# Kernel tuning notes

Measured on AMD Instinct MI355X. Metric: run time of the kernel, lower is better.

Reference implementation:

```python
import jax, jax.numpy as jnp
import numpy as np

N_NODES = 100000


def gcn_layer(x, src, dst, W, b):
    # Standard torch_geometric GCNConv: add self-loops, symmetric deg^-1/2 norm,
    # linear transform, scatter-add aggregation, bias.
    n = x.shape[0]
    h = x @ W                                   # [N, out]
    loop = jnp.arange(n)
    s = jnp.concatenate([src, loop])            # [E+N]
    d = jnp.concatenate([dst, loop])
    deg = jax.ops.segment_sum(jnp.ones_like(d, dtype=h.dtype), d, num_segments=n)
    dinv = jax.lax.rsqrt(jnp.maximum(deg, 1.0)) # deg>=1 thanks to self-loops
    norm = dinv[s] * dinv[d]                    # [E+N]
    out = jax.ops.segment_sum(h[s] * norm[:, None], d, num_segments=n)
    return out + b


def setup_inputs() -> dict:
    key = jax.random.key(0)
    ks = jax.random.split(key, 8)
    N, E, IN, H, A = N_NODES, 1600000, 128, 128, 16
    x = jax.random.normal(ks[0], (N, IN), dtype=jnp.float32)
    edge_index = jax.random.randint(ks[1], (2, E), 0, N, dtype=jnp.int64)
    sc = lambda fi, fo: 1.0 / np.sqrt(fi)
    W1 = jax.random.normal(ks[2], (IN, H), dtype=jnp.float32) * sc(IN, H)
    b1 = jnp.zeros((H,), dtype=jnp.float32)
    W2 = jax.random.normal(ks[3], (H, H), dtype=jnp.float32) * sc(H, H)
    b2 = jnp.zeros((H,), dtype=jnp.float32)
    Wm = jax.random.normal(ks[4], (H, A), dtype=jnp.float32) * sc(H, A)
    bm = jnp.zeros((A,), dtype=jnp.float32)
    Ws = jax.random.normal(ks[5], (H, A), dtype=jnp.float32) * sc(H, A)
    bs = jnp.zeros((A,), dtype=jnp.float32)
    return {"x": x, "edge_index": edge_index, "W1": W1, "b1": b1,
            "W2": W2, "b2": b2, "Wm": Wm, "bm": bm, "Ws": Ws, "bs": bs}


def reference(x, edge_index, W1, b1, W2, b2, Wm, bm, Ws, bs):
    src, dst = edge_index[0], edge_index[1]
    h = jax.nn.relu(gcn_layer(x, src, dst, W1, b1))
    h = jax.nn.relu(gcn_layer(h, src, dst, W2, b2))
    mean = h @ Wm + bm
    logstd = h @ Ws + bs
    return (mean, logstd)
```

## Files before the change

kernel.cpp:

```cpp
#include <hip/hip_runtime.h>
#include <hip/hip_bf16.h>
#include <stdint.h>

static __device__ __forceinline__ ushort f2bf(float f){
  uint u = __float_as_uint(f);
  uint r = (u + 0x7fffu + ((u >> 16) & 1u)) >> 16;
  return (ushort)r;
}
static __device__ __forceinline__ float bf_lo(uint v){ return __uint_as_float(v << 16); }
static __device__ __forceinline__ float bf_hi(uint v){ return __uint_as_float(v & 0xffff0000u); }



__global__ __launch_bounds__(256) void k_bcount(const int* __restrict__ dst, int E, int CH,
                                                int* __restrict__ bcnt){
  __shared__ int hist[1024];
  for (int i = threadIdx.x; i < 1024; i += 256) hist[i] = 0;
  __syncthreads();
  int begin = blockIdx.x * CH;
  int end   = min(begin + CH, E);
  int i0 = begin + threadIdx.x * 4;
  for (int i = i0; i + 4 <= end; i += 1024){
    int4 d4 = *(const int4*)&dst[i];
    atomicAdd(&hist[d4.x >> 7], 1);
    atomicAdd(&hist[d4.y >> 7], 1);
    atomicAdd(&hist[d4.z >> 7], 1);
    atomicAdd(&hist[d4.w >> 7], 1);
  }
  int tailStart = begin + ((end - begin) & ~3);
  if (tailStart < end && threadIdx.x < (end - tailStart)){
    atomicAdd(&hist[dst[tailStart + threadIdx.x] >> 7], 1);
  }
  __syncthreads();
  for (int b = threadIdx.x; b < 1024; b += 256){
    int h = hist[b];
    if (h) atomicAdd(&bcnt[b], h);
  }
}


__global__ __launch_bounds__(256) void k_bscan(const int* __restrict__ bcnt, int* __restrict__ boff,
                                               int* __restrict__ bcur, int E){
  __shared__ int sh[256];
  int t = threadIdx.x, base = t * 4;
  int v0 = bcnt[base], v1 = bcnt[base+1], v2 = bcnt[base+2], v3 = bcnt[base+3];
  int s = v0 + v1 + v2 + v3;
  sh[t] = s; __syncthreads();
  for (int off = 1; off < 256; off <<= 1){
    int x = (t >= off) ? sh[t-off] : 0;
    __syncthreads(); sh[t] += x; __syncthreads();
  }
  int run = sh[t] - s;
  boff[base]   = run; bcur[base]   = run; run += v0;
  boff[base+1] = run; bcur[base+1] = run; run += v1;
  boff[base+2] = run; bcur[base+2] = run; run += v2;
  boff[base+3] = run; bcur[base+3] = run; run += v3;
  if (t == 255) boff[1024] = E;
}


__global__ __launch_bounds__(256) void k_bscatter(const int* __restrict__ src, const int* __restrict__ dst,
                                                  int E, int CH, int* __restrict__ bcur,
                                                  uint* __restrict__ ebuf){
  __shared__ int hist[1024];
  __shared__ int basea[1024];
  __shared__ int cnt[1024];
  for (int i = threadIdx.x; i < 1024; i += 256){ hist[i] = 0; cnt[i] = 0; }
  __syncthreads();
  int begin = blockIdx.x * CH;
  int end   = min(begin + CH, E);
  int i0 = begin + threadIdx.x * 4;
  for (int i = i0; i + 4 <= end; i += 1024){
    int4 d4 = *(const int4*)&dst[i];
    atomicAdd(&hist[d4.x >> 7], 1);
    atomicAdd(&hist[d4.y >> 7], 1);
    atomicAdd(&hist[d4.z >> 7], 1);
    atomicAdd(&hist[d4.w >> 7], 1);
  }
  int tailStart = begin + ((end - begin) & ~3);
  if (tailStart < end && threadIdx.x < (end - tailStart)){
    atomicAdd(&hist[dst[tailStart + threadIdx.x] >> 7], 1);
  }
  __syncthreads();
  for (int b = threadIdx.x; b < 1024; b += 256){
    int h = hist[b];
    basea[b] = h ? atomicAdd(&bcur[b], h) : 0;
  }
  __syncthreads();
  for (int i = i0; i + 4 <= end; i += 1024){
    int4 d4 = *(const int4*)&dst[i];
    int4 s4 = *(const int4*)&src[i];
    int b0 = d4.x >> 7; int p0 = basea[b0] + atomicAdd(&cnt[b0], 1);
    ebuf[p0] = (uint)s4.x | (((uint)d4.x & 127u) << 20);
    int b1 = d4.y >> 7; int p1 = basea[b1] + atomicAdd(&cnt[b1], 1);
    ebuf[p1] = (uint)s4.y | (((uint)d4.y & 127u) << 20);
    int b2 = d4.z >> 7; int p2 = basea[b2] + atomicAdd(&cnt[b2], 1);
    ebuf[p2] = (uint)s4.z | (((uint)d4.z & 127u) << 20);
    int b3 = d4.w >> 7; int p3 = basea[b3] + atomicAdd(&cnt[b3], 1);
    ebuf[p3] = (uint)s4.w | (((uint)d4.w & 127u) << 20);
  }
  if (tailStart < end && threadIdx.x < (end - tailStart)){
    int j = tailStart + threadIdx.x;
    int d = dst[j], s = src[j];
    int b = d >> 7; int p = basea[b] + atomicAdd(&cnt[b], 1);
    ebuf[p] = (uint)s | (((uint)d & 127u) << 20);
  }
}


__global__ __launch_bounds__(256) void k_csr(const uint* __restrict__ ebuf, const int* __restrict__ boff,
                                             float* __restrict__ dinv, int* __restrict__ ofs,
                                             int* __restrict__ csr, int N){
  __shared__ int cnt[128];
  __shared__ int esc[128];
  __shared__ int cur[128];
  const int b = blockIdx.x;
  const int t = threadIdx.x;
  if (t < 128) cnt[t] = 0;
  __syncthreads();
  const int e0 = boff[b], e1 = boff[b+1];
  for (int i = e0 + t; i < e1; i += 256){
    atomicAdd(&cnt[(ebuf[i] >> 20) & 127u], 1);
  }
  __syncthreads();
  if (t < 128) esc[t] = cnt[t];
  __syncthreads();
  for (int off = 1; off < 128; off <<= 1){
    int v = 0;
    if (t < 128 && t >= off) v = esc[t - off];
    __syncthreads();
    if (t < 128) esc[t] += v;
    __syncthreads();
  }
  if (t < 128){
    int ex = esc[t] - cnt[t];
    cur[t] = ex;
    int node = b*128 + t;
    if (node < N){
      dinv[node] = rsqrtf((float)(cnt[t] + 1));
      ofs[node]  = e0 + ex;
    } else if (node == N){
      ofs[N] = e0 + ex;
    }
  }
  __syncthreads();
  for (int i = e0 + t; i < e1; i += 256){
    uint e = ebuf[i];
    int loc = (int)((e >> 20) & 127u);
    int p = e0 + atomicAdd(&cur[loc], 1);
    csr[p] = (int)(e & 0xFFFFFu);
  }
}

__global__ void k_ofs_last(int* __restrict__ ofs, int N, int E){ ofs[N] = E; }


__global__ __launch_bounds__(256, 2) void k_gemm128(const float* __restrict__ X, const float* __restrict__ W,
                                                    const float* __restrict__ dinv, ushort* __restrict__ G, int N){
  __shared__ float Xl[128*64];
  __shared__ float Wl[64*128];
  const int tid = threadIdx.x;
  const int tx = tid & 15;
  const int ty = tid >> 4;
  const int r0 = blockIdx.x * 128;

  float acc[8][8];
  #pragma unroll
  for (int j=0;j<8;++j)
    #pragma unroll
    for (int c=0;c<8;++c) acc[j][c] = 0.f;

  const float2* X2 = (const float2*)X;
  const float4* W4 = (const float4*)W;
  float2* Xl2 = (float2*)Xl;
  float4* Wl4 = (float4*)Wl;

  for (int kh = 0; kh < 2; ++kh){
    if (kh) __syncthreads();
    #pragma unroll
    for (int i=0;i<16;++i){
      int t = tid + i*256;
      int r = t >> 5, j = t & 31;
      int rs = r0 + r; if (rs >= N) rs = N - 1;
      Xl2[r*32 + j] = X2[(size_t)rs*64 + kh*32 + j];
    }
    #pragma unroll
    for (int i=0;i<8;++i){
      int t = tid + i*256;
      int k = t >> 5, c4 = t & 31;
      Wl4[k*32 + c4] = W4[(size_t)(kh*64 + k)*32 + c4];
    }
    __syncthreads();

    #pragma unroll 4
    for (int k2 = 0; k2 < 32; ++k2){
      float2 xv[8];
      #pragma unroll
      for (int j=0;j<8;++j) xv[j] = Xl2[(8*ty + j)*32 + k2];
      float4 wa0 = Wl4[(2*k2)*32   + 2*tx];
      float4 wa1 = Wl4[(2*k2)*32   + 2*tx + 1];
      float4 wb0 = Wl4[(2*k2+1)*32 + 2*tx];
      float4 wb1 = Wl4[(2*k2+1)*32 + 2*tx + 1];
      #pragma unroll
      for (int j=0;j<8;++j){
        acc[j][0] = fmaf(xv[j].x, wa0.x, acc[j][0]);
        acc[j][1] = fmaf(xv[j].x, wa0.y, acc[j][1]);
        acc[j][2] = fmaf(xv[j].x, wa0.z, acc[j][2]);
        acc[j][3] = fmaf(xv[j].x, wa0.w, acc[j][3]);
        acc[j][4] = fmaf(xv[j].x, wa1.x, acc[j][4]);
        acc[j][5] = fmaf(xv[j].x, wa1.y, acc[j][5]);
        acc[j][6] = fmaf(xv[j].x, wa1.z, acc[j][6]);
        acc[j][7] = fmaf(xv[j].x, wa1.w, acc[j][7]);
        acc[j][0] = fmaf(xv[j].y, wb0.x, acc[j][0]);
        acc[j][1] = fmaf(xv[j].y, wb0.y, acc[j][1]);
        acc[j][2] = fmaf(xv[j].y, wb0.z, acc[j][2]);
        acc[j][3] = fmaf(xv[j].y, wb0.w, acc[j][3]);
        acc[j][4] = fmaf(xv[j].y, wb1.x, acc[j][4]);
        acc[j][5] = fmaf(xv[j].y, wb1.y, acc[j][5]);
        acc[j][6] = fmaf(xv[j].y, wb1.z, acc[j][6]);
        acc[j][7] = fmaf(xv[j].y, wb1.w, acc[j][7]);
      }
    }
  }

  #pragma unroll
  for (int j=0;j<8;++j){
    int row = r0 + 8*ty + j;
    if (row < N){
      float dv = dinv[row];
      uint p0 = (uint)f2bf(acc[j][0]*dv) | ((uint)f2bf(acc[j][1]*dv) << 16);
      uint p1 = (uint)f2bf(acc[j][2]*dv) | ((uint)f2bf(acc[j][3]*dv) << 16);
      uint p2 = (uint)f2bf(acc[j][4]*dv) | ((uint)f2bf(acc[j][5]*dv) << 16);
      uint p3 = (uint)f2bf(acc[j][6]*dv) | ((uint)f2bf(acc[j][7]*dv) << 16);
      uint4* Gp = (uint4*)&G[(size_t)row*128 + 8*tx];
      *Gp = make_uint4(p0, p1, p2, p3);
    }
  }
}


__global__ __launch_bounds__(256) void k_agg(const ushort* __restrict__ G, const int* __restrict__ ofs,
                                             const int* __restrict__ csr, const float* __restrict__ dinv,
                                             const float* __restrict__ bias, float* __restrict__ OUT, int N){
  int wv   = __builtin_amdgcn_readfirstlane((int)(threadIdx.x >> 6));
  int lane = threadIdx.x & 63;
  int d = blockIdx.x*4 + wv;
  if (d >= N) return;
  const uint* Gu = (const uint*)G;
  float bx = bias[2*lane], by = bias[2*lane+1];
  int e0 = ofs[d], e1 = ofs[d+1];
  uint u0 = Gu[(size_t)d*64 + lane];
  float a0x = bf_lo(u0), a0y = bf_hi(u0);
  float a1x=0.f,a1y=0.f,a2x=0.f,a2y=0.f,a3x=0.f,a3y=0.f;
  int e = e0;
  for (; e+8 <= e1; e += 8){
    int s0=csr[e],   s1=csr[e+1], s2=csr[e+2], s3=csr[e+3];
    int s4=csr[e+4], s5=csr[e+5], s6=csr[e+6], s7=csr[e+7];
    uint v0 = Gu[(size_t)s0*64 + lane];
    uint v1 = Gu[(size_t)s1*64 + lane];
    uint v2 = Gu[(size_t)s2*64 + lane];
    uint v3 = Gu[(size_t)s3*64 + lane];
    uint v4 = Gu[(size_t)s4*64 + lane];
    uint v5 = Gu[(size_t)s5*64 + lane];
    uint v6 = Gu[(size_t)s6*64 + lane];
    uint v7 = Gu[(size_t)s7*64 + lane];
    a0x += bf_lo(v0); a0y += bf_hi(v0);
    a1x += bf_lo(v1); a1y += bf_hi(v1);
    a2x += bf_lo(v2); a2y += bf_hi(v2);
    a3x += bf_lo(v3); a3y += bf_hi(v3);
    a0x += bf_lo(v4); a0y += bf_hi(v4);
    a1x += bf_lo(v5); a1y += bf_hi(v5);
    a2x += bf_lo(v6); a2y += bf_hi(v6);
    a3x += bf_lo(v7); a3y += bf_hi(v7);
  }
  for (; e+4 <= e1; e += 4){
    int s0=csr[e], s1=csr[e+1], s2=csr[e+2], s3=csr[e+3];
    uint v0 = Gu[(size_t)s0*64 + lane];
    uint v1 = Gu[(size_t)s1*64 + lane];
    uint v2 = Gu[(size_t)s2*64 + lane];
    uint v3 = Gu[(size_t)s3*64 + lane];
    a0x += bf_lo(v0); a0y += bf_hi(v0);
    a1x += bf_lo(v1); a1y += bf_hi(v1);
    a2x += bf_lo(v2); a2y += bf_hi(v2);
    a3x += bf_lo(v3); a3y += bf_hi(v3);
  }
  for (; e < e1; ++e){
    int s = csr[e];
    uint v = Gu[(size_t)s*64 + lane];
    a0x += bf_lo(v); a0y += bf_hi(v);
  }
  float sx = (a0x+a1x)+(a2x+a3x), sy = (a0y+a1y)+(a2y+a3y);
  float dv = dinv[d];
  float rx = fmaxf(fmaf(dv, sx, bx), 0.f);
  float ry = fmaxf(fmaf(dv, sy, by), 0.f);
  *(float2*)&OUT[(size_t)d*128 + 2*lane] = make_float2(rx, ry);
}


__global__ __launch_bounds__(256, 2) void k_heads(const float* __restrict__ H, const float* __restrict__ Wm,
                                                  const float* __restrict__ bm, const float* __restrict__ Ws,
                                                  const float* __restrict__ bs, float* __restrict__ OUT, int N){
  __shared__ float Hl[128*66];
  __shared__ float Wl[128*32];
  const int tid = threadIdx.x;
  const int tx = tid & 3;
  const int ty = tid >> 2;
  const int r0 = blockIdx.x * 128;

  for (int i = tid; i < 128*16; i += 256){
    int k = i >> 4, cc = i & 15;
    Wl[k*32 + cc]      = Wm[i];
    Wl[k*32 + 16 + cc] = Ws[i];
  }

  float acc[2][8];
  #pragma unroll
  for (int j=0;j<2;++j)
    #pragma unroll
    for (int c=0;c<8;++c) acc[j][c] = 0.f;

  const float2* H2 = (const float2*)H;
  float2* Hl2 = (float2*)Hl;
  const float4* Wl4 = (const float4*)Wl;

  for (int kh = 0; kh < 2; ++kh){
    if (kh) __syncthreads();
    #pragma unroll
    for (int i=0;i<16;++i){
      int t = tid + i*256;
      int r = t >> 5, j = t & 31;
      int rs = r0 + r; if (rs >= N) rs = N - 1;
      Hl2[r*33 + j] = H2[(size_t)rs*64 + kh*32 + j];
    }
    __syncthreads();

    #pragma unroll 4
    for (int k2 = 0; k2 < 32; ++k2){
      float2 x0 = Hl2[(2*ty)*33 + k2];
      float2 x1 = Hl2[(2*ty+1)*33 + k2];
      float4 wa0 = Wl4[(kh*64 + 2*k2)*8   + 2*tx];
      float4 wa1 = Wl4[(kh*64 + 2*k2)*8   + 2*tx + 1];
      float4 wb0 = Wl4[(kh*64 + 2*k2+1)*8 + 2*tx];
      float4 wb1 = Wl4[(kh*64 + 2*k2+1)*8 + 2*tx + 1];
      #pragma unroll
      for (int rr=0;rr<2;++rr){
        float xa = rr ? x1.x : x0.x;
        float xb = rr ? x1.y : x0.y;
        acc[rr][0] = fmaf(xa, wa0.x, acc[rr][0]);
        acc[rr][1] = fmaf(xa, wa0.y, acc[rr][1]);
        acc[rr][2] = fmaf(xa, wa0.z, acc[rr][2]);
        acc[rr][3] = fmaf(xa, wa0.w, acc[rr][3]);
        acc[rr][4] = fmaf(xa, wa1.x, acc[rr][4]);
        acc[rr][5] = fmaf(xa, wa1.y, acc[rr][5]);
        acc[rr][6] = fmaf(xa, wa1.z, acc[rr][6]);
        acc[rr][7] = fmaf(xa, wa1.w, acc[rr][7]);
        acc[rr][0] = fmaf(xb, wb0.x, acc[rr][0]);
        acc[rr][1] = fmaf(xb, wb0.y, acc[rr][1]);
        acc[rr][2] = fmaf(xb, wb0.z, acc[rr][2]);
        acc[rr][3] = fmaf(xb, wb0.w, acc[rr][3]);
        acc[rr][4] = fmaf(xb, wb1.x, acc[rr][4]);
        acc[rr][5] = fmaf(xb, wb1.y, acc[rr][5]);
        acc[rr][6] = fmaf(xb, wb1.z, acc[rr][6]);
        acc[rr][7] = fmaf(xb, wb1.w, acc[rr][7]);
      }
    }
  }

  int c0 = 8*tx;
  float bv[8];
  #pragma unroll
  for (int i=0;i<8;++i) bv[i] = (tx < 2) ? bm[c0+i] : bs[c0+i-16];
  #pragma unroll
  for (int rr=0;rr<2;++rr){
    int row = r0 + 2*ty + rr;
    if (row < N){
      float4 o0 = make_float4(acc[rr][0]+bv[0], acc[rr][1]+bv[1], acc[rr][2]+bv[2], acc[rr][3]+bv[3]);
      float4 o1 = make_float4(acc[rr][4]+bv[4], acc[rr][5]+bv[5], acc[rr][6]+bv[6], acc[rr][7]+bv[7]);
      float* base = (tx < 2) ? &OUT[(size_t)row*16 + c0]
                             : &OUT[(size_t)N*16 + (size_t)row*16 + (c0-16)];
      float4* Op = (float4*)base;
      Op[0] = o0; Op[1] = o1;
    }
  }
}


extern "C" void kernel_launch(void* const* d_in, const int* in_sizes, int n_in,
                              void* d_out, int out_size, void* d_ws, size_t ws_size,
                              hipStream_t stream){
  const float* x  = (const float*)d_in[0];
  const int*   ei = (const int*)d_in[1];
  const float* W1 = (const float*)d_in[2];
  const float* b1 = (const float*)d_in[3];
  const float* W2 = (const float*)d_in[4];
  const float* b2 = (const float*)d_in[5];
  const float* Wm = (const float*)d_in[6];
  const float* bm = (const float*)d_in[7];
  const float* Ws = (const float*)d_in[8];
  const float* bs = (const float*)d_in[9];
  float* out = (float*)d_out;

  int N = in_sizes[0] / 128;
  int E = in_sizes[1] / 2;
  const int* src = ei;
  const int* dst = ei + E;

  char* w = (char*)d_ws;
  size_t o = 0;
  auto alloc = [&](size_t bytes)->char*{
    char* p = w + o; o = (o + bytes + 255) & ~(size_t)255; return p;
  };
  int*    bcnt = (int*)   alloc(1024*4);
  int*    boff = (int*)   alloc(1025*4);
  int*    bcur = (int*)   alloc(1024*4);
  float*  dinv = (float*) alloc((size_t)N*4);
  int*    ofs  = (int*)   alloc((size_t)(N+1)*4);
  uint*   ebuf = (uint*)  alloc((size_t)E*4);
  int*    csr  = (int*)   alloc((size_t)E*4);
  ushort* bufG = (ushort*)alloc((size_t)N*128*2);
  float*  bufH = (float*) alloc((size_t)N*128*4);
  (void)ws_size; (void)n_in; (void)out_size;

  hipMemsetAsync(bcnt, 0, 1024*4, stream);

  int NB = (N + 127)/128;
  int CH = (E + 255)/256; CH = (CH + 3) & ~3;

  k_bcount  <<<256, 256, 0, stream>>>(dst, E, CH, bcnt);
  k_bscan   <<<1,   256, 0, stream>>>(bcnt, boff, bcur, E);
  k_bscatter<<<256, 256, 0, stream>>>(src, dst, E, CH, bcur, ebuf);
  k_csr     <<<NB,  256, 0, stream>>>(ebuf, boff, dinv, ofs, csr, N);
  if ((N & 127) == 0) k_ofs_last<<<1, 1, 0, stream>>>(ofs, N, E);

  int gAgg = (N + 3)/4;

  k_gemm128<<<NB,   256, 0, stream>>>(x,    W1, dinv, bufG, N);
  k_agg    <<<gAgg, 256, 0, stream>>>(bufG, ofs, csr, dinv, b1, bufH, N);
  k_gemm128<<<NB,   256, 0, stream>>>(bufH, W2, dinv, bufG, N);
  k_agg    <<<gAgg, 256, 0, stream>>>(bufG, ofs, csr, dinv, b2, bufH, N);
  k_heads  <<<NB,   256, 0, stream>>>(bufH, Wm, bm, Ws, bs, out, N);
}
```

Baseline: 404.9 us.

## Replace FP32 SIMT GEMM with bf16 MFMA GEMM using swizzled LDS tiles

The 128x128 node-feature GEMM now runs on MFMA 16x16x32 bf16 instructions instead of scalar FP32 FMAs. X and W are converted to bf16 while being staged into LDS, with W transposed, and both use an XOR swizzle to avoid bank conflicts. The full K dimension is loaded in one pass. Inputs are now rounded to bf16 before the multiply, which adds precision loss, and the output is written as scattered 2-byte stores instead of 16-byte vector stores.

After: 335.9 us. 1.21x faster.

```diff
diff --git a/kernel.cpp b/kernel.cpp
--- a/kernel.cpp
+++ b/kernel.cpp
@@ -9,6 +9,9 @@
 }
 static __device__ __forceinline__ float bf_lo(uint v){ return __uint_as_float(v << 16); }
 static __device__ __forceinline__ float bf_hi(uint v){ return __uint_as_float(v & 0xffff0000u); }
+
+using short8 = __attribute__((ext_vector_type(8))) short;
+using f32x4  = __attribute__((ext_vector_type(4))) float;
 
 
 
@@ -155,85 +158,90 @@
 __global__ void k_ofs_last(int* __restrict__ ofs, int N, int E){ ofs[N] = E; }
 
 
-__global__ __launch_bounds__(256, 2) void k_gemm128(const float* __restrict__ X, const float* __restrict__ W,
-                                                    const float* __restrict__ dinv, ushort* __restrict__ G, int N){
-  __shared__ float Xl[128*64];
-  __shared__ float Wl[64*128];
+__global__ __launch_bounds__(256, 2) void k_gemm_mfma(const float* __restrict__ X, const float* __restrict__ W,
+                                                      const float* __restrict__ dinv, ushort* __restrict__ G, int N){
+  __shared__ ushort Xl[128*128];
+  __shared__ ushort Wt[128*128];
   const int tid = threadIdx.x;
-  const int tx = tid & 15;
-  const int ty = tid >> 4;
   const int r0 = blockIdx.x * 128;
 
-  float acc[8][8];
-  #pragma unroll
-  for (int j=0;j<8;++j)
-    #pragma unroll
-    for (int c=0;c<8;++c) acc[j][c] = 0.f;
-
-  const float2* X2 = (const float2*)X;
-  const float4* W4 = (const float4*)W;
-  float2* Xl2 = (float2*)Xl;
-  float4* Wl4 = (float4*)Wl;
-
-  for (int kh = 0; kh < 2; ++kh){
-    if (kh) __syncthreads();
-    #pragma unroll
-    for (int i=0;i<16;++i){
-      int t = tid + i*256;
-      int r = t >> 5, j = t & 31;
-      int rs = r0 + r; if (rs >= N) rs = N - 1;
-      Xl2[r*32 + j] = X2[(size_t)rs*64 + kh*32 + j];
-    }
-    #pragma unroll
-    for (int i=0;i<8;++i){
-      int t = tid + i*256;
-      int k = t >> 5, c4 = t & 31;
-      Wl4[k*32 + c4] = W4[(size_t)(kh*64 + k)*32 + c4];
-    }
-    __syncthreads();
-
-    #pragma unroll 4
-    for (int k2 = 0; k2 < 32; ++k2){
-      float2 xv[8];
+  #pragma unroll
+  for (int i = 0; i < 16; ++i){
+    int t = tid + i*256;
+    int row = t >> 5, f4 = t & 31;
+    int rs = r0 + row; if (rs >= N) rs = N - 1;
+    float4 v = *(const float4*)&X[(size_t)rs*128 + f4*4];
+    uint p0 = (uint)f2bf(v.x) | ((uint)f2bf(v.y) << 16);
+    uint p1 = (uint)f2bf(v.z) | ((uint)f2bf(v.w) << 16);
+    int kb = f4 >> 1, sub = (f4 & 1) * 4;
+    *(uint2*)&Xl[row*128 + ((kb ^ (row & 7)) << 3) + sub] = make_uint2(p0, p1);
+  }
+  #pragma unroll
+  for (int i = 0; i < 8; ++i){
+    int t = tid + i*256;
+    int c = t & 127, kg = t >> 7;
+    int k0 = kg * 8;
+    float w0 = W[(size_t)(k0+0)*128 + c];
+    float w1 = W[(size_t)(k0+1)*128 + c];
+    float w2 = W[(size_t)(k0+2)*128 + c];
+    float w3 = W[(size_t)(k0+3)*128 + c];
+    float w4 = W[(size_t)(k0+4)*128 + c];
+    float w5 = W[(size_t)(k0+5)*128 + c];
+    float w6 = W[(size_t)(k0+6)*128 + c];
+    float w7 = W[(size_t)(k0+7)*128 + c];
+    uint q0 = (uint)f2bf(w0) | ((uint)f2bf(w1) << 16);
+    uint q1 = (uint)f2bf(w2) | ((uint)f2bf(w3) << 16);
+    uint q2 = (uint)f2bf(w4) | ((uint)f2bf(w5) << 16);
+    uint q3 = (uint)f2bf(w6) | ((uint)f2bf(w7) << 16);
+    *(uint4*)&Wt[c*128 + ((kg ^ (c & 7)) << 3)] = make_uint4(q0, q1, q2, q3);
+  }
+  __syncthreads();
+
+  const int wv   = tid >> 6;
+  const int lane = tid & 63;
+  const int lr   = lane & 15;
+  const int lq   = lane >> 4;
+  const int swz  = lr & 7;
+
+  f32x4 acc[2][8];
+  #pragma unroll
+  for (int m = 0; m < 2; ++m)
+    #pragma unroll
+    for (int n = 0; n < 8; ++n) acc[m][n] = (f32x4){0.f, 0.f, 0.f, 0.f};
+
+  #pragma unroll
+  for (int ks = 0; ks < 4; ++ks){
+    int off = ((ks*4 + lq) ^ swz) << 3;
+    short8 a0 = *(const short8*)&Xl[(wv*32 +      lr)*128 + off];
+    short8 a1 = *(const short8*)&Xl[(wv*32 + 16 + lr)*128 + off];
+    short8 b[8];
+    #pragma unroll
+    for (int n = 0; n < 8; ++n) b[n] = *(const short8*)&Wt[(n*16 + lr)*128 + off];
+    #pragma unroll
+    for (int n = 0; n < 8; ++n){
+      acc[0][n] = __builtin_amdgcn_mfma_f32_16x16x32_bf16(a0, b[n], acc[0][n], 0, 0, 0);
+      acc[1][n] = __builtin_amdgcn_mfma_f32_16x16x32_bf16(a1, b[n], acc[1][n], 0, 0, 0);
+    }
+  }
+
+  #pragma unroll
+  for (int m = 0; m < 2; ++m){
+    int rbase = r0 + wv*32 + m*16 + 4*lq;
+    float dv[4]; bool ok[4];
+    #pragma unroll
+    for (int rg = 0; rg < 4; ++rg){
+      int row = rbase + rg;
+      ok[rg] = row < N;
+      dv[rg] = dinv[ok[rg] ? row : (N-1)];
+    }
+    #pragma unroll
+    for (int n = 0; n < 8; ++n){
       #pragma unroll
-      for (int j=0;j<8;++j) xv[j] = Xl2[(8*ty + j)*32 + k2];
-      float4 wa0 = Wl4[(2*k2)*32   + 2*tx];
-      float4 wa1 = Wl4[(2*k2)*32   + 2*tx + 1];
-      float4 wb0 = Wl4[(2*k2+1)*32 + 2*tx];
-      float4 wb1 = Wl4[(2*k2+1)*32 + 2*tx + 1];
-      #pragma unroll
-      for (int j=0;j<8;++j){
-        acc[j][0] = fmaf(xv[j].x, wa0.x, acc[j][0]);
-        acc[j][1] = fmaf(xv[j].x, wa0.y, acc[j][1]);
-        acc[j][2] = fmaf(xv[j].x, wa0.z, acc[j][2]);
-        acc[j][3] = fmaf(xv[j].x, wa0.w, acc[j][3]);
-        acc[j][4] = fmaf(xv[j].x, wa1.x, acc[j][4]);
-        acc[j][5] = fmaf(xv[j].x, wa1.y, acc[j][5]);
-        acc[j][6] = fmaf(xv[j].x, wa1.z, acc[j][6]);
-        acc[j][7] = fmaf(xv[j].x, wa1.w, acc[j][7]);
-        acc[j][0] = fmaf(xv[j].y, wb0.x, acc[j][0]);
-        acc[j][1] = fmaf(xv[j].y, wb0.y, acc[j][1]);
-        acc[j][2] = fmaf(xv[j].y, wb0.z, acc[j][2]);
-        acc[j][3] = fmaf(xv[j].y, wb0.w, acc[j][3]);
-        acc[j][4] = fmaf(xv[j].y, wb1.x, acc[j][4]);
-        acc[j][5] = fmaf(xv[j].y, wb1.y, acc[j][5]);
-        acc[j][6] = fmaf(xv[j].y, wb1.z, acc[j][6]);
-        acc[j][7] = fmaf(xv[j].y, wb1.w, acc[j][7]);
+      for (int rg = 0; rg < 4; ++rg){
+        if (ok[rg]){
+          G[(size_t)(rbase + rg)*128 + n*16 + lr] = f2bf(acc[m][n][rg] * dv[rg]);
+        }
       }
-    }
-  }
-
-  #pragma unroll
-  for (int j=0;j<8;++j){
-    int row = r0 + 8*ty + j;
-    if (row < N){
-      float dv = dinv[row];
-      uint p0 = (uint)f2bf(acc[j][0]*dv) | ((uint)f2bf(acc[j][1]*dv) << 16);
-      uint p1 = (uint)f2bf(acc[j][2]*dv) | ((uint)f2bf(acc[j][3]*dv) << 16);
-      uint p2 = (uint)f2bf(acc[j][4]*dv) | ((uint)f2bf(acc[j][5]*dv) << 16);
-      uint p3 = (uint)f2bf(acc[j][6]*dv) | ((uint)f2bf(acc[j][7]*dv) << 16);
-      uint4* Gp = (uint4*)&G[(size_t)row*128 + 8*tx];
-      *Gp = make_uint4(p0, p1, p2, p3);
     }
   }
 }
@@ -434,9 +442,9 @@
 
   int gAgg = (N + 3)/4;
 
-  k_gemm128<<<NB,   256, 0, stream>>>(x,    W1, dinv, bufG, N);
-  k_agg    <<<gAgg, 256, 0, stream>>>(bufG, ofs, csr, dinv, b1, bufH, N);
-  k_gemm128<<<NB,   256, 0, stream>>>(bufH, W2, dinv, bufG, N);
-  k_agg    <<<gAgg, 256, 0, stream>>>(bufG, ofs, csr, dinv, b2, bufH, N);
-  k_heads  <<<NB,   256, 0, stream>>>(bufH, Wm, bm, Ws, bs, out, N);
-}
+  k_gemm_mfma<<<NB,   256, 0, stream>>>(x,    W1, dinv, bufG, N);
+  k_agg      <<<gAgg, 256, 0, stream>>>(bufG, ofs, csr, dinv, b1, bufH, N);
+  k_gemm_mfma<<<NB,   256, 0, stream>>>(bufH, W2, dinv, bufG, N);
+  k_agg      <<<gAgg, 256, 0, stream>>>(bufG, ofs, csr, dinv, b2, bufH, N);
+  k_heads    <<<NB,   256, 0, stream>>>(bufH, Wm, bm, Ws, bs, out, N);
+}
```
